# Kernel tuning notes

Measured on AMD Instinct MI355X. Metric: run time of the kernel, lower is better.

The kernel has to match this reference:

```python
import jax, jax.numpy as jnp
import numpy as np
from jax import lax

T, B, IN, H, OUT = 128, 256, 512, 512, 10


def spike(x):
    # spikingjelly heaviside spike: 1 if x >= 0 else 0
    return (x >= 0).astype(x.dtype)


def setup_inputs() -> dict:
    key = jax.random.key(0)
    ks = jax.random.split(key, 7)
    s_ih = 1.0 / np.sqrt(IN)
    s_hh = 1.0 / np.sqrt(H)
    return {
        "x": jax.random.normal(ks[0], (T, B, IN), jnp.float32),
        "w_ih": jax.random.uniform(ks[1], (4 * H, IN), jnp.float32, -s_ih, s_ih),
        "b_ih": jax.random.uniform(ks[2], (4 * H,), jnp.float32, -s_ih, s_ih),
        "w_hh": jax.random.uniform(ks[3], (4 * H, H), jnp.float32, -s_hh, s_hh),
        "b_hh": jax.random.uniform(ks[4], (4 * H,), jnp.float32, -s_hh, s_hh),
        "fc_w": jax.random.uniform(ks[5], (OUT, H), jnp.float32, -s_hh, s_hh),
        "fc_b": jax.random.uniform(ks[6], (OUT,), jnp.float32, -s_hh, s_hh),
    }


def reference(x, w_ih, b_ih, w_hh, b_hh, fc_w, fc_b):
    # precompute input projection for all timesteps: [T, B, 4H]
    xg = jnp.einsum('tbi,gi->tbg', x, w_ih) + b_ih
    h0 = jnp.zeros((B, H), x.dtype)
    c0 = jnp.zeros((B, H), x.dtype)

    def step(carry, xg_t):
        h, c = carry
        gates = xg_t + h @ w_hh.T + b_hh  # [B, 4H]
        i, f, g, o = jnp.split(gates, 4, axis=-1)
        i, f, g, o = spike(i), spike(f), spike(g), spike(o)
        c = f * c + i * g
        h = c * o  # spiking LSTM: no tanh on cell
        return (h, c), None

    (h, c), _ = lax.scan(step, (h0, c0), xg)
    logits = h @ fc_w.T + fc_b  # last timestep hidden -> [B, OUT]
    return jax.nn.softmax(logits, axis=1)
```

## Files before the change

kernel.cpp:

```cpp
#include <hip/hip_runtime.h>
#include <math.h>

#define NB 256
#define NH 512
#define NIN 512
#define NT 128
#define NG 2048

__device__ float g_h0[NB * NH];
__device__ float g_h1[NB * NH];
__device__ float g_xg[(size_t)NT * NB * NG];
#define FLAG_STRIDE 32
__device__ int g_flags[256 * FLAG_STRIDE];

#define WSTR 516
#define HSTR 68
#define LDS_WF (64 * WSTR)
#define LDS_HF (2 * 32 * HSTR)
#define LDS_BYTES ((LDS_WF + LDS_HF) * 4)

__global__ __launch_bounds__(256) void zero_state() {
    int i = blockIdx.x * 256 + threadIdx.x;
    g_h0[i] = 0.f;
    if (i < 256 * FLAG_STRIDE) g_flags[i] = 0;
}

#define BM 128
#define BN 128
#define BK 16

__global__ __launch_bounds__(256, 2) void xg_gemm(
    const float* __restrict__ x,
    const float* __restrict__ w_ih)
{
    __shared__ float As[2][BK][BM + 4];
    __shared__ float Bs[2][BK][BN + 4];

    const int tid = threadIdx.x;
    const int bm = blockIdx.x >> 4;
    const int bn = blockIdx.x & 15;
    const size_t m0 = (size_t)bm * BM;
    const int n0 = bn * BN;

    const int srow = tid >> 1;
    const int sc4  = (tid & 1) * 8;
    const float* __restrict__ Arow = x    + (m0 + srow) * NIN;
    const float* __restrict__ Brow = w_ih + (size_t)(n0 + srow) * NIN;

    const int tx = tid & 15;
    const int ty = tid >> 4;

    float acc[8][8];
    #pragma unroll
    for (int i = 0; i < 8; ++i)
        #pragma unroll
        for (int j = 0; j < 8; ++j) acc[i][j] = 0.f;

    float4 ar0, ar1, br0, br1;

#define LOAD_TILE(kb) do {                                   \
        ar0 = *(const float4*)(Arow + (kb) + sc4);           \
        ar1 = *(const float4*)(Arow + (kb) + sc4 + 4);       \
        br0 = *(const float4*)(Brow + (kb) + sc4);           \
        br1 = *(const float4*)(Brow + (kb) + sc4 + 4);       \
    } while (0)

#define STORE_TILE(buf) do {                                             \
        As[buf][sc4+0][srow] = ar0.x; As[buf][sc4+1][srow] = ar0.y;      \
        As[buf][sc4+2][srow] = ar0.z; As[buf][sc4+3][srow] = ar0.w;      \
        As[buf][sc4+4][srow] = ar1.x; As[buf][sc4+5][srow] = ar1.y;      \
        As[buf][sc4+6][srow] = ar1.z; As[buf][sc4+7][srow] = ar1.w;      \
        Bs[buf][sc4+0][srow] = br0.x; Bs[buf][sc4+1][srow] = br0.y;      \
        Bs[buf][sc4+2][srow] = br0.z; Bs[buf][sc4+3][srow] = br0.w;      \
        Bs[buf][sc4+4][srow] = br1.x; Bs[buf][sc4+5][srow] = br1.y;      \
        Bs[buf][sc4+6][srow] = br1.z; Bs[buf][sc4+7][srow] = br1.w;      \
    } while (0)

    auto mk = [&](int buf) {
        #pragma unroll
        for (int k = 0; k < BK; ++k) {
            const float4 a0 = *(const float4*)(&As[buf][k][ty * 4]);
            const float4 a1 = *(const float4*)(&As[buf][k][64 + ty * 4]);
            const float4 b0 = *(const float4*)(&Bs[buf][k][tx * 4]);
            const float4 b1 = *(const float4*)(&Bs[buf][k][64 + tx * 4]);
            const float av[8] = {a0.x, a0.y, a0.z, a0.w, a1.x, a1.y, a1.z, a1.w};
            const float bv[8] = {b0.x, b0.y, b0.z, b0.w, b1.x, b1.y, b1.z, b1.w};
            #pragma unroll
            for (int i = 0; i < 8; ++i)
                #pragma unroll
                for (int j = 0; j < 8; ++j)
                    acc[i][j] = fmaf(av[i], bv[j], acc[i][j]);
        }
    };

    LOAD_TILE(0);
    STORE_TILE(0);
    __syncthreads();
    for (int tt = 0; tt < 31; ++tt) {
        LOAD_TILE((tt + 1) * BK);
        mk(tt & 1);
        STORE_TILE((tt + 1) & 1);
        __syncthreads();
    }
    mk(1);

    #pragma unroll
    for (int i = 0; i < 8; ++i) {
        const int mr = (i < 4) ? (ty * 4 + i) : (64 + ty * 4 + i - 4);
        float* __restrict__ orow = g_xg + (m0 + mr) * NG + n0;
        *(float4*)(orow + tx * 4)      = make_float4(acc[i][0], acc[i][1], acc[i][2], acc[i][3]);
        *(float4*)(orow + 64 + tx * 4) = make_float4(acc[i][4], acc[i][5], acc[i][6], acc[i][7]);
    }
#undef LOAD_TILE
#undef STORE_TILE
}

__global__ __launch_bounds__(256) void lstm_persist(
    const float* __restrict__ w_hh,
    const float* __restrict__ b_ih,
    const float* __restrict__ b_hh)
{
    extern __shared__ float smem[];
    float* __restrict__ Wl = smem;
    float* __restrict__ Hl = smem + LDS_WF;

    const int tid = threadIdx.x;
    const int grp = blockIdx.x & 7;
    const int jb  = blockIdx.x >> 3;
    const int j0 = jb * 16;
    const int b0 = grp * 32;

    {
        const int wr = tid >> 2;
        const int wf = tid & 3;
        const int wq = wr >> 4, wjl = wr & 15;
        const float* __restrict__ Wrow = w_hh + (size_t)(wq * NH + j0 + wjl) * NH;
        for (int kb = 0; kb < 512; kb += 128) {
            #pragma unroll
            for (int i = 0; i < 8; ++i) {
                float4 v = *(const float4*)(Wrow + kb + (wf + 4 * i) * 4);
                *(float4*)(&Wl[wr * WSTR + kb + (wf + 4 * i) * 4]) = v;
            }
        }
    }

    const int jj = tid & 15;
    const int bg = tid >> 4;
    const int hr = tid >> 3;
    const int hc = tid & 7;

    float bi[4], bh[4];
    #pragma unroll
    for (int q = 0; q < 4; ++q) {
        const int g = q * NH + j0 + jj;
        bi[q] = b_ih[g];
        bh[q] = b_hh[g];
    }

    float cc[2] = {0.f, 0.f};
    float* h_in  = g_h0;
    float* h_out = g_h1;

    int* __restrict__ my_flag   = &g_flags[(size_t)blockIdx.x * FLAG_STRIDE];
    int* __restrict__ poll_flag = (tid < 32)
        ? &g_flags[(size_t)((tid << 3) | grp) * FLAG_STRIDE] : nullptr;

    float xgc[2][4];
    {
        const size_t base = ((size_t)b0 + bg * 2) * NG + j0 + jj;
        #pragma unroll
        for (int q = 0; q < 4; ++q) xgc[0][q] = g_xg[base + (size_t)q * NH];
        #pragma unroll
        for (int q = 0; q < 4; ++q) xgc[1][q] = g_xg[base + NG + (size_t)q * NH];
    }

    for (int t = 0; t < NT; ++t) {
        float acc[2][4];
        #pragma unroll
        for (int ib = 0; ib < 2; ++ib)
            #pragma unroll
            for (int q = 0; q < 4; ++q) acc[ib][q] = 0.f;

        float* Hrow = h_in + (size_t)(b0 + hr) * NH;
        float hreg[8];
        auto hload = [&](int kb) {
            #pragma unroll
            for (int u = 0; u < 4; ++u)
                hreg[u] = __hip_atomic_load(&Hrow[kb + hc * 4 + u],
                                            __ATOMIC_RELAXED, __HIP_MEMORY_SCOPE_AGENT);
            #pragma unroll
            for (int u = 0; u < 4; ++u)
                hreg[4 + u] = __hip_atomic_load(&Hrow[kb + (hc + 8) * 4 + u],
                                                __ATOMIC_RELAXED, __HIP_MEMORY_SCOPE_AGENT);
        };
        auto hstore = [&](int buf) {
            *(float4*)(&Hl[buf * 32 * HSTR + hr * HSTR + hc * 4]) =
                make_float4(hreg[0], hreg[1], hreg[2], hreg[3]);
            *(float4*)(&Hl[buf * 32 * HSTR + hr * HSTR + (hc + 8) * 4]) =
                make_float4(hreg[4], hreg[5], hreg[6], hreg[7]);
        };
        auto mk = [&](int buf, int kc) {
            #pragma unroll
            for (int kk = 0; kk < 64; kk += 4) {
                const float4 h0v = *(const float4*)(&Hl[buf * 32 * HSTR + (bg * 2 + 0) * HSTR + kk]);
                const float4 h1v = *(const float4*)(&Hl[buf * 32 * HSTR + (bg * 2 + 1) * HSTR + kk]);
                #pragma unroll
                for (int q = 0; q < 4; ++q) {
                    const float4 w4 = *(const float4*)(&Wl[(q * 16 + jj) * WSTR + kc + kk]);
                    float a0 = acc[0][q], a1 = acc[1][q];
                    a0 = fmaf(h0v.x, w4.x, a0); a1 = fmaf(h1v.x, w4.x, a1);
                    a0 = fmaf(h0v.y, w4.y, a0); a1 = fmaf(h1v.y, w4.y, a1);
                    a0 = fmaf(h0v.z, w4.z, a0); a1 = fmaf(h1v.z, w4.z, a1);
                    a0 = fmaf(h0v.w, w4.w, a0); a1 = fmaf(h1v.w, w4.w, a1);
                    acc[0][q] = a0; acc[1][q] = a1;
                }
            }
        };

        hload(0);

        float xgn[2][4];
        {
            const int tp = (t < NT - 1) ? t + 1 : t;
            const size_t base = ((size_t)tp * NB + b0 + bg * 2) * NG + j0 + jj;
            #pragma unroll
            for (int q = 0; q < 4; ++q) xgn[0][q] = g_xg[base + (size_t)q * NH];
            #pragma unroll
            for (int q = 0; q < 4; ++q) xgn[1][q] = g_xg[base + NG + (size_t)q * NH];
        }

        hstore(0);
        __syncthreads();
        for (int tc = 0; tc < 7; ++tc) {
            hload((tc + 1) * 64);
            mk(tc & 1, tc * 64);
            hstore((tc + 1) & 1);
            __syncthreads();
        }
        mk(1, 448);

        #pragma unroll
        for (int ib = 0; ib < 2; ++ib) {
            float s[4];
            #pragma unroll
            for (int q = 0; q < 4; ++q) {
                const float gate = ((xgc[ib][q] + bi[q]) + acc[ib][q]) + bh[q];
                s[q] = (gate >= 0.0f) ? 1.f : 0.f;
            }
            cc[ib] = s[1] * cc[ib] + s[0] * s[2];
            __hip_atomic_store(&h_out[(size_t)(b0 + bg * 2 + ib) * NH + j0 + jj],
                               cc[ib] * s[3],
                               __ATOMIC_RELAXED, __HIP_MEMORY_SCOPE_AGENT);
        }

        #pragma unroll
        for (int ib = 0; ib < 2; ++ib)
            #pragma unroll
            for (int q = 0; q < 4; ++q) xgc[ib][q] = xgn[ib][q];

        float* tin = h_in; h_in = h_out; h_out = tin;

        if (t != NT - 1) {
            __syncthreads();
            if (tid == 0)
                __hip_atomic_store(my_flag, t + 1,
                                   __ATOMIC_RELAXED, __HIP_MEMORY_SCOPE_AGENT);
            if (tid < 32) {
                while (__hip_atomic_load(poll_flag,
                                         __ATOMIC_RELAXED, __HIP_MEMORY_SCOPE_AGENT) < t + 1)
                    __builtin_amdgcn_s_sleep(1);
            }
            __syncthreads();
        }
    }
}

__global__ __launch_bounds__(64) void final2(
    const float* __restrict__ fc_w,
    const float* __restrict__ fc_b,
    float* __restrict__ out)
{
    __shared__ float hl[NH];
    __shared__ float ls[10];
    const int b = blockIdx.x;
    const int tid = threadIdx.x;
    const float* __restrict__ hb = g_h0 + (size_t)b * NH;
    *(float4*)(&hl[tid * 4])       = *(const float4*)(hb + tid * 4);
    *(float4*)(&hl[256 + tid * 4]) = *(const float4*)(hb + 256 + tid * 4);
    __syncthreads();
    if (tid < 10) {
        float a = 0.f;
        const float* __restrict__ wr = fc_w + (size_t)tid * NH;
        for (int j = 0; j < NH; j += 4) {
            const float4 w4 = *(const float4*)(wr + j);
            a = fmaf(hl[j + 0], w4.x, a);
            a = fmaf(hl[j + 1], w4.y, a);
            a = fmaf(hl[j + 2], w4.z, a);
            a = fmaf(hl[j + 3], w4.w, a);
        }
        ls[tid] = a + fc_b[tid];
    }
    __syncthreads();
    if (tid == 0) {
        float m = -3.4e38f;
        #pragma unroll
        for (int o = 0; o < 10; ++o) m = (ls[o] > m) ? ls[o] : m;
        float e[10], ssum = 0.f;
        #pragma unroll
        for (int o = 0; o < 10; ++o) { e[o] = expf(ls[o] - m); ssum += e[o]; }
        const float inv = 1.0f / ssum;
        #pragma unroll
        for (int o = 0; o < 10; ++o) out[b * 10 + o] = e[o] * inv;
    }
}

extern "C" void kernel_launch(void* const* d_in, const int* in_sizes, int n_in,
                              void* d_out, int out_size, void* d_ws, size_t ws_size,
                              hipStream_t stream) {
    const float* x    = (const float*)d_in[0];
    const float* w_ih = (const float*)d_in[1];
    const float* b_ih = (const float*)d_in[2];
    const float* w_hh = (const float*)d_in[3];
    const float* b_hh = (const float*)d_in[4];
    const float* fc_w = (const float*)d_in[5];
    const float* fc_b = (const float*)d_in[6];
    float* out = (float*)d_out;

    static bool attr_set = false;
    if (!attr_set) {
        hipFuncSetAttribute((const void*)lstm_persist,
                            hipFuncAttributeMaxDynamicSharedMemorySize, LDS_BYTES);
        attr_set = true;
    }

    zero_state<<<512, 256, 0, stream>>>();

    xg_gemm<<<4096, 256, 0, stream>>>(x, w_ih);

    lstm_persist<<<256, 256, LDS_BYTES, stream>>>(w_hh, b_ih, b_hh);

    final2<<<256, 64, 0, stream>>>(fc_w, fc_b, out);
}
```

Baseline: 3.030 ms.

## Replace block-wide barriers with per-wavefront flags and drop intra-step syncthreads

Each wavefront's hidden-state rows in LDS are written and read only by that same wavefront, so the in-loop `__syncthreads` calls are removed. The cross-block step barrier now uses one flag per wavefront. Each wave publishes its own progress after a `vmcnt(0)` wait and polls the matching waves of the blocks in its batch group using a wave-wide `__all` vote. The aim is to let waves proceed independently instead of waiting on the slowest wave in the block. The cost is four times more flag traffic, plus reliance on wavefront lockstep and on relaxed atomics for LDS and global visibility.

```diff
diff --git a/kernel.cpp b/kernel.cpp
--- a/kernel.cpp
+++ b/kernel.cpp
@@ -7,11 +7,13 @@
 #define NT 128
 #define NG 2048
 
+typedef __attribute__((ext_vector_type(4))) float f32x4;
+
 __device__ float g_h0[NB * NH];
 __device__ float g_h1[NB * NH];
 __device__ float g_xg[(size_t)NT * NB * NG];
 #define FLAG_STRIDE 32
-__device__ int g_flags[256 * FLAG_STRIDE];
+__device__ int g_flags[256 * 4 * FLAG_STRIDE];
 
 #define WSTR 516
 #define HSTR 68
@@ -22,7 +24,7 @@
 __global__ __launch_bounds__(256) void zero_state() {
     int i = blockIdx.x * 256 + threadIdx.x;
     g_h0[i] = 0.f;
-    if (i < 256 * FLAG_STRIDE) g_flags[i] = 0;
+    if (i < 256 * 4 * FLAG_STRIDE) g_flags[i] = 0;
 }
 
 #define BM 128
@@ -129,6 +131,8 @@
     const int jb  = blockIdx.x >> 3;
     const int j0 = jb * 16;
     const int b0 = grp * 32;
+    const int lane = tid & 63;
+    const int wv   = tid >> 6;
 
     {
         const int wr = tid >> 2;
@@ -143,6 +147,7 @@
             }
         }
     }
+    __syncthreads();
 
     const int jj = tid & 15;
     const int bg = tid >> 4;
@@ -158,12 +163,10 @@
     }
 
     float cc[2] = {0.f, 0.f};
-    float* h_in  = g_h0;
-    float* h_out = g_h1;
-
-    int* __restrict__ my_flag   = &g_flags[(size_t)blockIdx.x * FLAG_STRIDE];
-    int* __restrict__ poll_flag = (tid < 32)
-        ? &g_flags[(size_t)((tid << 3) | grp) * FLAG_STRIDE] : nullptr;
+
+    int* __restrict__ my_flag = &g_flags[((size_t)blockIdx.x * 4 + wv) * FLAG_STRIDE];
+    int* __restrict__ poll_flag =
+        &g_flags[(((size_t)((lane & 31) << 3) | grp) * 4 + wv) * FLAG_STRIDE];
 
     float xgc[2][4];
     {
@@ -181,7 +184,9 @@
             #pragma unroll
             for (int q = 0; q < 4; ++q) acc[ib][q] = 0.f;
 
-        float* Hrow = h_in + (size_t)(b0 + hr) * NH;
+        const float* h_in = (t & 1) ? g_h1 : g_h0;
+        const float* Hrow = h_in + (size_t)(b0 + hr) * NH;
+
         float hreg[8];
         auto hload = [&](int kb) {
             #pragma unroll
@@ -194,10 +199,10 @@
                                                 __ATOMIC_RELAXED, __HIP_MEMORY_SCOPE_AGENT);
         };
         auto hstore = [&](int buf) {
-            *(float4*)(&Hl[buf * 32 * HSTR + hr * HSTR + hc * 4]) =
-                make_float4(hreg[0], hreg[1], hreg[2], hreg[3]);
-            *(float4*)(&Hl[buf * 32 * HSTR + hr * HSTR + (hc + 8) * 4]) =
-                make_float4(hreg[4], hreg[5], hreg[6], hreg[7]);
+            float* d = &Hl[buf * 32 * HSTR + hr * HSTR + hc * 4];
+            *(f32x4*)(d)     = *(f32x4*)(&hreg[0]);
+            float* d2 = &Hl[buf * 32 * HSTR + hr * HSTR + (hc + 8) * 4];
+            *(f32x4*)(d2)    = *(f32x4*)(&hreg[4]);
         };
         auto mk = [&](int buf, int kc) {
             #pragma unroll
@@ -230,15 +235,14 @@
         }
 
         hstore(0);
-        __syncthreads();
         for (int tc = 0; tc < 7; ++tc) {
             hload((tc + 1) * 64);
             mk(tc & 1, tc * 64);
             hstore((tc + 1) & 1);
-            __syncthreads();
         }
         mk(1, 448);
 
+        float* hout = ((t & 1) ? g_h0 : g_h1) + (size_t)b0 * NH;
         #pragma unroll
         for (int ib = 0; ib < 2; ++ib) {
             float s[4];
@@ -248,7 +252,7 @@
                 s[q] = (gate >= 0.0f) ? 1.f : 0.f;
             }
             cc[ib] = s[1] * cc[ib] + s[0] * s[2];
-            __hip_atomic_store(&h_out[(size_t)(b0 + bg * 2 + ib) * NH + j0 + jj],
+            __hip_atomic_store(hout + (size_t)(bg * 2 + ib) * NH + j0 + jj,
                                cc[ib] * s[3],
                                __ATOMIC_RELAXED, __HIP_MEMORY_SCOPE_AGENT);
         }
@@ -258,19 +262,19 @@
             #pragma unroll
             for (int q = 0; q < 4; ++q) xgc[ib][q] = xgn[ib][q];
 
-        float* tin = h_in; h_in = h_out; h_out = tin;
-
         if (t != NT - 1) {
-            __syncthreads();
-            if (tid == 0)
+            asm volatile("s_waitcnt vmcnt(0)" ::: "memory");
+            if (lane == 0)
                 __hip_atomic_store(my_flag, t + 1,
                                    __ATOMIC_RELAXED, __HIP_MEMORY_SCOPE_AGENT);
-            if (tid < 32) {
-                while (__hip_atomic_load(poll_flag,
-                                         __ATOMIC_RELAXED, __HIP_MEMORY_SCOPE_AGENT) < t + 1)
-                    __builtin_amdgcn_s_sleep(1);
+            const int need = t + 1;
+            while (true) {
+                const int v = (lane < 32)
+                    ? __hip_atomic_load(poll_flag, __ATOMIC_RELAXED, __HIP_MEMORY_SCOPE_AGENT)
+                    : need;
+                if (__all(v >= need)) break;
+                __builtin_amdgcn_s_sleep(1);
             }
-            __syncthreads();
         }
     }
 }
```

New measurement: 2.978 ms. No clear change (-1.7%).
